# Optimization experiments

Hardware: AMD Instinct MI355X
Metric: run time of the kernel (lower is better)

## Reference

```python
import jax, jax.numpy as jnp
import numpy as np

D_MODEL = 2048
NUM_EXPERTS = 64
TOP_K = 2
EPS = 1e-8


def setup_inputs() -> dict:
    key = jax.random.key(0)
    kx, kw = jax.random.split(key)
    x = jax.random.normal(kx, (32768, D_MODEL), dtype=jnp.float32)
    # nn.Linear(d_model, num_experts, bias=False) weight: [E, D], init std=0.02
    gate_w = jax.random.normal(kw, (NUM_EXPERTS, D_MODEL), dtype=jnp.float32) * 0.02
    expert_bias = jnp.zeros((NUM_EXPERTS,), dtype=jnp.float32)  # buffer, zeros at init
    return {"x": x, "gate_w": gate_w, "expert_bias": expert_bias}


def reference(x, gate_w, expert_bias):
    # logits = x @ W^T + bias  : [N, E]
    logits = jnp.einsum("nd,ed->ne", x, gate_w) + expert_bias
    routing_probs = jax.nn.softmax(logits, axis=-1)
    # top-k over experts, then renormalize selected weights
    routing_weights, selected_experts = jax.lax.top_k(routing_probs, TOP_K)
    routing_weights = routing_weights / (
        jnp.sum(routing_weights, axis=-1, keepdims=True) + EPS
    )
    return routing_weights, selected_experts
```

## Files before the change

### kernel.cpp

```cpp
#include <hip/hip_runtime.h>
#include <math.h>

#define D_MODEL 2048
#define NEXP    64
#define NROWS   32768
#define BM      64
#define BK      16
#define PAD     4
#define LDX     (BM + PAD)

__global__ __launch_bounds__(256, 2) void router_kernel(
    const float* __restrict__ x,
    const float* __restrict__ gw,
    const float* __restrict__ bias,
    float* __restrict__ out)
{
    __shared__ alignas(16) float xs[BK][LDX];
    __shared__ alignas(16) float ws[BK][LDX];
    __shared__ float logits[BM][NEXP + 1];

    const int t  = threadIdx.x;
    const int b  = blockIdx.x;
    const int r0 = b * BM;

    const int rg  = t & 15;
    const int eg  = t >> 4;
    const int rg4 = rg * 4;
    const int eg4 = eg * 4;

    const int sr  = t >> 2;
    const int skq = t & 3;
    const float* xrow = x  + (size_t)(r0 + sr) * D_MODEL + skq * 4;
    const float* wrow = gw + (size_t)sr        * D_MODEL + skq * 4;

    float acc[4][4];
#pragma unroll
    for (int i = 0; i < 4; ++i)
#pragma unroll
        for (int j = 0; j < 4; ++j) acc[i][j] = 0.f;

    float4 xv = *(const float4*)(xrow);
    float4 wv = *(const float4*)(wrow);

    for (int k0 = 0; k0 < D_MODEL; k0 += BK) {
        __syncthreads();
        {
            const int kq4 = skq * 4;
            xs[kq4 + 0][sr] = xv.x; xs[kq4 + 1][sr] = xv.y;
            xs[kq4 + 2][sr] = xv.z; xs[kq4 + 3][sr] = xv.w;
            ws[kq4 + 0][sr] = wv.x; ws[kq4 + 1][sr] = wv.y;
            ws[kq4 + 2][sr] = wv.z; ws[kq4 + 3][sr] = wv.w;
        }
        __syncthreads();

        if (k0 + BK < D_MODEL) {
            xv = *(const float4*)(xrow + k0 + BK);
            wv = *(const float4*)(wrow + k0 + BK);
        }

#pragma unroll
        for (int k = 0; k < BK; ++k) {
            const float4 xq = *(const float4*)&xs[k][rg4];
            const float4 wq = *(const float4*)&ws[k][eg4];
            acc[0][0] = fmaf(xq.x, wq.x, acc[0][0]);
            acc[0][1] = fmaf(xq.x, wq.y, acc[0][1]);
            acc[0][2] = fmaf(xq.x, wq.z, acc[0][2]);
            acc[0][3] = fmaf(xq.x, wq.w, acc[0][3]);
            acc[1][0] = fmaf(xq.y, wq.x, acc[1][0]);
            acc[1][1] = fmaf(xq.y, wq.y, acc[1][1]);
            acc[1][2] = fmaf(xq.y, wq.z, acc[1][2]);
            acc[1][3] = fmaf(xq.y, wq.w, acc[1][3]);
            acc[2][0] = fmaf(xq.z, wq.x, acc[2][0]);
            acc[2][1] = fmaf(xq.z, wq.y, acc[2][1]);
            acc[2][2] = fmaf(xq.z, wq.z, acc[2][2]);
            acc[2][3] = fmaf(xq.z, wq.w, acc[2][3]);
            acc[3][0] = fmaf(xq.w, wq.x, acc[3][0]);
            acc[3][1] = fmaf(xq.w, wq.y, acc[3][1]);
            acc[3][2] = fmaf(xq.w, wq.z, acc[3][2]);
            acc[3][3] = fmaf(xq.w, wq.w, acc[3][3]);
        }
    }

    __syncthreads();
#pragma unroll
    for (int i = 0; i < 4; ++i)
#pragma unroll
        for (int j = 0; j < 4; ++j)
            logits[rg4 + i][eg4 + j] = acc[i][j];
    __syncthreads();

    if (t < BM) {
        const int row = r0 + t;
        float m1 = -INFINITY, m2 = -INFINITY;
        int   e1 = 0, e2 = 0;
        for (int e = 0; e < NEXP; ++e) {
            const float l = logits[t][e] + bias[e];
            if (l > m1) { m2 = m1; e2 = e1; m1 = l; e1 = e; }
            else if (l > m2) { m2 = l; e2 = e; }
        }
        float z = 0.f;
        for (int e = 0; e < NEXP; ++e)
            z += expf(logits[t][e] + bias[e] - m1);
        const float p2    = expf(m2 - m1);
        const float denom = (1.f + p2) + 1e-8f * z;
        out[row * 2 + 0] = 1.f / denom;
        out[row * 2 + 1] = p2 / denom;
        float* oidx = out + 2 * NROWS;
        oidx[row * 2 + 0] = (float)e1;
        oidx[row * 2 + 1] = (float)e2;
    }
}

extern "C" void kernel_launch(void* const* d_in, const int* in_sizes, int n_in,
                              void* d_out, int out_size, void* d_ws, size_t ws_size,
                              hipStream_t stream) {
    const float* x    = (const float*)d_in[0];
    const float* gw   = (const float*)d_in[1];
    const float* bias = (const float*)d_in[2];
    float* out = (float*)d_out;
    (void)in_sizes; (void)n_in; (void)out_size; (void)d_ws; (void)ws_size;

    dim3 grid(NROWS / BM);
    dim3 block(256);
    router_kernel<<<grid, block, 0, stream>>>(x, gw, bias, out);
}
```

Before: 407.6 us.

## Stage x via direct global-to-LDS loads and read gate weights from global

Restructures the GEMM so each of 8 waves owns 8 experts and each lane owns one row. x tiles are staged into double-buffered LDS with global_load_lds (async, bypassing registers), and the 64x2048 gate weights are read straight from global memory as wave-uniform vectors, so they are likely served from cache. This removes the register round-trip and the LDS transpose stores of the old scheme and uses 512-thread blocks. It risks heavy redundant weight traffic through the caches and lower arithmetic intensity per thread, since each thread holds only 8 accumulators.

```diff
diff --git a/kernel.cpp b/kernel.cpp
--- a/kernel.cpp
+++ b/kernel.cpp
@@ -5,88 +5,88 @@
 #define NEXP    64
 #define NROWS   32768
 #define BM      64
-#define BK      16
-#define PAD     4
-#define LDX     (BM + PAD)
+#define BK      64
+#define NCHUNK  (D_MODEL / BK)
+#define NGRAN   (BK / 4)
 
-__global__ __launch_bounds__(256, 2) void router_kernel(
+typedef float f32x8 __attribute__((ext_vector_type(8)));
+
+__device__ __forceinline__ void stage16(const float* gsrc, void* lds_base) {
+    __builtin_amdgcn_global_load_lds(
+        (const __attribute__((address_space(1))) void*)gsrc,
+        (__attribute__((address_space(3))) void*)lds_base,
+        16, 0, 0);
+}
+
+#define ROW_FMA(J, WV)                           \
+    acc[J] = fmaf(WV[0], xa.x, acc[J]);          \
+    acc[J] = fmaf(WV[1], xa.y, acc[J]);          \
+    acc[J] = fmaf(WV[2], xa.z, acc[J]);          \
+    acc[J] = fmaf(WV[3], xa.w, acc[J]);          \
+    acc[J] = fmaf(WV[4], xb.x, acc[J]);          \
+    acc[J] = fmaf(WV[5], xb.y, acc[J]);          \
+    acc[J] = fmaf(WV[6], xb.z, acc[J]);          \
+    acc[J] = fmaf(WV[7], xb.w, acc[J]);
+
+__global__ __launch_bounds__(512, 4) void router_kernel(
     const float* __restrict__ x,
     const float* __restrict__ gw,
     const float* __restrict__ bias,
     float* __restrict__ out)
 {
-    __shared__ alignas(16) float xs[BK][LDX];
-    __shared__ alignas(16) float ws[BK][LDX];
-    __shared__ float logits[BM][NEXP + 1];
+    __shared__ alignas(16) float4 xsg[2][NGRAN][BM];
+    __shared__ alignas(16) float  logits[BM][68];
 
-    const int t  = threadIdx.x;
-    const int b  = blockIdx.x;
-    const int r0 = b * BM;
+    const int t    = threadIdx.x;
+    const int lane = t & 63;
+    const int w    = __builtin_amdgcn_readfirstlane(t >> 6);
+    const int r0   = blockIdx.x * BM;
 
-    const int rg  = t & 15;
-    const int eg  = t >> 4;
-    const int rg4 = rg * 4;
-    const int eg4 = eg * 4;
+    const float* wp   = gw + (size_t)(w * 8) * D_MODEL;
+    const float* xrow = x  + (size_t)(r0 + lane) * D_MODEL;
+    const int q0 = w * 2;
 
-    const int sr  = t >> 2;
-    const int skq = t & 3;
-    const float* xrow = x  + (size_t)(r0 + sr) * D_MODEL + skq * 4;
-    const float* wrow = gw + (size_t)sr        * D_MODEL + skq * 4;
+    float acc[8];
+#pragma unroll
+    for (int j = 0; j < 8; ++j) acc[j] = 0.f;
 
-    float acc[4][4];
+    stage16(xrow + q0 * 4,     &xsg[0][q0][0]);
+    stage16(xrow + q0 * 4 + 4, &xsg[0][q0 + 1][0]);
+    __syncthreads();
+
+    for (int c = 0; c < NCHUNK; ++c) {
+        const int cur = c & 1;
+        if (c + 1 < NCHUNK) {
+            const int kb2 = (c + 1) * BK;
+            stage16(xrow + kb2 + q0 * 4,     &xsg[cur ^ 1][q0][0]);
+            stage16(xrow + kb2 + q0 * 4 + 4, &xsg[cur ^ 1][q0 + 1][0]);
+        }
+        const int kb = c * BK;
 #pragma unroll
-    for (int i = 0; i < 4; ++i)
-#pragma unroll
-        for (int j = 0; j < 4; ++j) acc[i][j] = 0.f;
-
-    float4 xv = *(const float4*)(xrow);
-    float4 wv = *(const float4*)(wrow);
-
-    for (int k0 = 0; k0 < D_MODEL; k0 += BK) {
-        __syncthreads();
-        {
-            const int kq4 = skq * 4;
-            xs[kq4 + 0][sr] = xv.x; xs[kq4 + 1][sr] = xv.y;
-            xs[kq4 + 2][sr] = xv.z; xs[kq4 + 3][sr] = xv.w;
-            ws[kq4 + 0][sr] = wv.x; ws[kq4 + 1][sr] = wv.y;
-            ws[kq4 + 2][sr] = wv.z; ws[kq4 + 3][sr] = wv.w;
+        for (int g = 0; g < NGRAN; g += 2) {
+            const f32x8 w0 = *(const f32x8*)(wp + 0 * D_MODEL + kb + g * 4);
+            const f32x8 w1 = *(const f32x8*)(wp + 1 * D_MODEL + kb + g * 4);
+            const f32x8 w2 = *(const f32x8*)(wp + 2 * D_MODEL + kb + g * 4);
+            const f32x8 w3 = *(const f32x8*)(wp + 3 * D_MODEL + kb + g * 4);
+            const f32x8 w4 = *(const f32x8*)(wp + 4 * D_MODEL + kb + g * 4);
+            const f32x8 w5 = *(const f32x8*)(wp + 5 * D_MODEL + kb + g * 4);
+            const f32x8 w6 = *(const f32x8*)(wp + 6 * D_MODEL + kb + g * 4);
+            const f32x8 w7 = *(const f32x8*)(wp + 7 * D_MODEL + kb + g * 4);
+            const float4 xa = xsg[cur][g][lane];
+            const float4 xb = xsg[cur][g + 1][lane];
+            ROW_FMA(0, w0) ROW_FMA(1, w1) ROW_FMA(2, w2) ROW_FMA(3, w3)
+            ROW_FMA(4, w4) ROW_FMA(5, w5) ROW_FMA(6, w6) ROW_FMA(7, w7)
         }
         __syncthreads();
-
-        if (k0 + BK < D_MODEL) {
-            xv = *(const float4*)(xrow + k0 + BK);
-            wv = *(const float4*)(wrow + k0 + BK);
-        }
-
-#pragma unroll
-        for (int k = 0; k < BK; ++k) {
-            const float4 xq = *(const float4*)&xs[k][rg4];
-            const float4 wq = *(const float4*)&ws[k][eg4];
-            acc[0][0] = fmaf(xq.x, wq.x, acc[0][0]);
-            acc[0][1] = fmaf(xq.x, wq.y, acc[0][1]);
-            acc[0][2] = fmaf(xq.x, wq.z, acc[0][2]);
-            acc[0][3] = fmaf(xq.x, wq.w, acc[0][3]);
-            acc[1][0] = fmaf(xq.y, wq.x, acc[1][0]);
-            acc[1][1] = fmaf(xq.y, wq.y, acc[1][1]);
-            acc[1][2] = fmaf(xq.y, wq.z, acc[1][2]);
-            acc[1][3] = fmaf(xq.y, wq.w, acc[1][3]);
-            acc[2][0] = fmaf(xq.z, wq.x, acc[2][0]);
-            acc[2][1] = fmaf(xq.z, wq.y, acc[2][1]);
-            acc[2][2] = fmaf(xq.z, wq.z, acc[2][2]);
-            acc[2][3] = fmaf(xq.z, wq.w, acc[2][3]);
-            acc[3][0] = fmaf(xq.w, wq.x, acc[3][0]);
-            acc[3][1] = fmaf(xq.w, wq.y, acc[3][1]);
-            acc[3][2] = fmaf(xq.w, wq.z, acc[3][2]);
-            acc[3][3] = fmaf(xq.w, wq.w, acc[3][3]);
-        }
     }
 
-    __syncthreads();
-#pragma unroll
-    for (int i = 0; i < 4; ++i)
-#pragma unroll
-        for (int j = 0; j < 4; ++j)
-            logits[rg4 + i][eg4 + j] = acc[i][j];
+    {
+        float4 lo, hi;
+        lo.x = acc[0]; lo.y = acc[1]; lo.z = acc[2]; lo.w = acc[3];
+        hi.x = acc[4]; hi.y = acc[5]; hi.z = acc[6]; hi.w = acc[7];
+        *(float4*)&logits[lane][w * 8]     = lo;
+        *(float4*)&logits[lane][w * 8 + 4] = hi;
+    }
     __syncthreads();
 
     if (t < BM) {
@@ -121,6 +121,6 @@
     (void)in_sizes; (void)n_in; (void)out_size; (void)d_ws; (void)ws_size;
 
     dim3 grid(NROWS / BM);
-    dim3 block(256);
+    dim3 block(512);
     router_kernel<<<grid, block, 0, stream>>>(x, gw, bias, out);
 }
```

After: 702.8 us. 1.72x slower.
